# Kernel tuning notes

Hardware: AMD Instinct MI355X
Metric: run time of the kernel (lower is better)

The kernel has to match this reference:

```python
import jax, jax.numpy as jnp
import numpy as np

B, T, C = 8, 4096, 1024
NH = 64          # module sets self.n_head = dim_head = 64
HD = C // NH     # 16


def setup_inputs() -> dict:
    key = jax.random.key(0)
    ks = jax.random.split(key, 9)
    s = 1.0 / np.sqrt(C).astype(np.float32)
    x = jax.random.normal(ks[0], (B, T, C), jnp.float32)
    Wq = jax.random.normal(ks[1], (C, C), jnp.float32) * s
    bq = jax.random.normal(ks[2], (C,), jnp.float32) * 0.01
    Wk = jax.random.normal(ks[3], (C, C), jnp.float32) * s
    bk = jax.random.normal(ks[4], (C,), jnp.float32) * 0.01
    Wv = jax.random.normal(ks[5], (C, C), jnp.float32) * s
    bv = jax.random.normal(ks[6], (C,), jnp.float32) * 0.01
    Wp = jax.random.normal(ks[7], (C, C), jnp.float32) * s
    bp = jax.random.normal(ks[8], (C,), jnp.float32) * 0.01
    return {"x": x, "Wq": Wq, "bq": bq, "Wk": Wk, "bk": bk,
            "Wv": Wv, "bv": bv, "Wp": Wp, "bp": bp}


def _heads(t):
    # [B, T, C] -> [B, NH, T, HD]
    return t.reshape(B, T, NH, HD).transpose(0, 2, 1, 3)


def reference(x, Wq, bq, Wk, bk, Wv, bv, Wp, bp):
    # self-attention path: y = x; kv_mask=None (masked path is unreachable in source)
    q = _heads(x @ Wq.T + bq)
    k = _heads(x @ Wk.T + bk)
    v = _heads(x @ Wv.T + bv)
    q = jax.nn.softmax(q, axis=-1)
    k = jax.nn.softmax(k, axis=-1)
    k_cumsum = k.sum(axis=2, keepdims=True)               # [B, NH, 1, HD]
    D_inv = 1.0 / (q * k_cumsum).sum(axis=-1, keepdims=True)  # [B, NH, T, 1]
    context = jnp.einsum('bhtd,bhte->bhde', k, v)          # [B, NH, HD, HD]
    y = jnp.einsum('bhtd,bhde->bhte', q, context) * D_inv  # [B, NH, T, HD]
    y = y.transpose(0, 2, 1, 3).reshape(B, T, C)           # b h n d -> b n (h d)
    return y @ Wp.T + bp
```

## Files before the change

kernel.cpp:

```cpp
#include <hip/hip_runtime.h>
#include <stdint.h>


typedef __attribute__((ext_vector_type(8))) __bf16 bf16x8;
typedef __attribute__((ext_vector_type(4))) float f32x4;
typedef __attribute__((ext_vector_type(4))) unsigned int u32x4;
typedef __attribute__((ext_vector_type(4))) unsigned short u16x4;

#define AS1 __attribute__((address_space(1)))
#define AS3 __attribute__((address_space(3)))

__device__ __forceinline__ unsigned short f2bf(float f) {
  unsigned int u = __builtin_bit_cast(unsigned int, f);
  u += 0x7FFFu + ((u >> 16) & 1u);
  return (unsigned short)(u >> 16);
}

__device__ __forceinline__ void gl_lds16(const unsigned short* g, unsigned short* l) {
  __builtin_amdgcn_global_load_lds((const AS1 unsigned int*)g, (AS3 unsigned int*)l, 16, 0, 0);
}

__global__ __launch_bounds__(256)
void cvt_x(const float* __restrict__ src, unsigned short* __restrict__ dst, int n4) {
  int i = blockIdx.x * blockDim.x + threadIdx.x;
  const int stride = gridDim.x * blockDim.x;
  for (; i < n4; i += stride) {
    f32x4 v = *(const f32x4*)(src + (size_t)i * 4);
    u16x4 o;
    o.x = f2bf(v.x); o.y = f2bf(v.y); o.z = f2bf(v.z); o.w = f2bf(v.w);
    *(u16x4*)(dst + (size_t)i * 4) = o;
  }
}

__global__ __launch_bounds__(256)
void cvt_w(const float* __restrict__ w0, const float* __restrict__ w1,
           const float* __restrict__ w2, const float* __restrict__ w3,
           unsigned short* __restrict__ dst) {
  const int j = blockIdx.x * 256 + threadIdx.x;
  const float* ws[4] = {w0, w1, w2, w3};
  #pragma unroll
  for (int r = 0; r < 4; ++r) {
    f32x4 v = *(const f32x4*)(ws[r] + (size_t)j * 4);
    u16x4 o;
    o.x = f2bf(v.x); o.y = f2bf(v.y); o.z = f2bf(v.z); o.w = f2bf(v.w);
    *(u16x4*)(dst + ((size_t)r * 262144 + j) * 4) = o;
  }
}

template<int KIND>
__global__ __launch_bounds__(256, 3)
void gemm_pipe(const unsigned short* __restrict__ A,
               const unsigned short* __restrict__ W,
               const float* __restrict__ b0, const float* __restrict__ b1,
               const float* __restrict__ b2,
               unsigned short* __restrict__ oq, unsigned short* __restrict__ okT,
               unsigned short* __restrict__ ovT, float* __restrict__ of)
{
  __shared__ __align__(16) unsigned short lds[24576];

  const int tid  = threadIdx.x;
  const int lane = tid & 63;
  const int wid  = tid >> 6;

  const int flat  = blockIdx.x;
  const int xcd   = flat & 7;
  const int i     = flat >> 3;
  const int bcg   = i >> 8;
  const int r     = i & 255;
  const int panel = r >> 3;
  const int c     = r & 7;
  const int brow  = (xcd * 32 + panel) * 128;
  const int bcol  = (bcg * 8 + c) * 128;

  const int srow = wid * 16 + (lane >> 2);
  const int scol = ((lane & 3) ^ ((lane >> 3) & 3)) << 3;
  const unsigned short* a_src = A + (size_t)(brow + srow) * 1024 + scol;
  const unsigned short* b_src = W + (size_t)(bcol + srow) * 1024 + scol;
  unsigned short* Ldst = lds + wid * 512;

  const int wm = (wid >> 1) * 64;
  const int wn = (wid & 1) * 64;
  const int fr = lane & 15;
  const int fg = lane >> 4;
  const int sw = ((fg ^ ((fr >> 1) & 3)) << 3);
  const int aoff = (wm + fr) * 32 + sw;
  const int boff = 4096 + (wn + fr) * 32 + sw;

  const f32x4 fz = {0.f, 0.f, 0.f, 0.f};
  f32x4 acc[4][4];
  #pragma unroll
  for (int mt = 0; mt < 4; ++mt)
    #pragma unroll
    for (int nt = 0; nt < 4; ++nt) acc[mt][nt] = fz;

  auto stage = [&](int t, int buf) {
    unsigned short* d = Ldst + buf * 8192;
    const unsigned short* ga = a_src + t * 32;
    const unsigned short* gb = b_src + t * 32;
    gl_lds16(ga,         d);
    gl_lds16(ga + 65536, d + 2048);
    gl_lds16(gb,         d + 4096);
    gl_lds16(gb + 65536, d + 6144);
  };

  stage(0, 0);
  stage(1, 1);
  stage(2, 2);
  asm volatile("s_waitcnt vmcnt(8)" ::: "memory");
  __builtin_amdgcn_sched_barrier(0);
  __builtin_amdgcn_s_barrier();

  int buf = 0;
  for (int t = 0; t < 32; ++t) {
    const unsigned short* Lb = lds + buf * 8192;
    bf16x8 af[4], bfr[4];
    #pragma unroll
    for (int mt = 0; mt < 4; ++mt)
      af[mt] = __builtin_bit_cast(bf16x8, *(const u32x4*)&Lb[aoff + mt * 512]);
    #pragma unroll
    for (int nt = 0; nt < 4; ++nt)
      bfr[nt] = __builtin_bit_cast(bf16x8, *(const u32x4*)&Lb[boff + nt * 512]);
    asm volatile("s_waitcnt lgkmcnt(0)" ::: "memory");
    __builtin_amdgcn_sched_barrier(0);
    __builtin_amdgcn_s_barrier();
    if (t < 29) stage(t + 3, buf);

    __builtin_amdgcn_s_setprio(1);
    #pragma unroll
    for (int mt = 0; mt < 4; ++mt)
      #pragma unroll
      for (int nt = 0; nt < 4; ++nt)
        acc[mt][nt] = __builtin_amdgcn_mfma_f32_16x16x32_bf16(af[mt], bfr[nt], acc[mt][nt], 0, 0, 0);
    __builtin_amdgcn_s_setprio(0);

    if (t < 29) {
      asm volatile("s_waitcnt vmcnt(8)" ::: "memory");
      __builtin_amdgcn_sched_barrier(0);
      __builtin_amdgcn_s_barrier();
    } else if (t == 29) {
      asm volatile("s_waitcnt vmcnt(4)" ::: "memory");
      __builtin_amdgcn_sched_barrier(0);
      __builtin_amdgcn_s_barrier();
    } else if (t == 30) {
      asm volatile("s_waitcnt vmcnt(0)" ::: "memory");
      __builtin_amdgcn_sched_barrier(0);
      __builtin_amdgcn_s_barrier();
    }
    buf = (buf == 2) ? 0 : buf + 1;
  }

  const int sec = (KIND == 0) ? (bcol >> 10) : 0;
  const float* bias = (KIND == 1) ? b0 : (sec == 0 ? b0 : (sec == 1 ? b1 : b2));

  #pragma unroll
  for (int nt = 0; nt < 4; ++nt) {
    const int n_glob = bcol + wn + nt * 16 + fr;
    const int nn = (KIND == 0) ? (n_glob & 1023) : n_glob;
    const float bv = bias[nn];
    #pragma unroll
    for (int mt = 0; mt < 4; ++mt) {
      const int m0 = brow + wm + mt * 16 + fg * 4;
      float vals[4];
      #pragma unroll
      for (int r2 = 0; r2 < 4; ++r2) vals[r2] = acc[mt][nt][r2] + bv;

      if (KIND == 0 && sec <= 1) {
        #pragma unroll
        for (int r2 = 0; r2 < 4; ++r2) {
          float x = vals[r2];
          float mx = x;
          #pragma unroll
          for (int s = 1; s < 16; s <<= 1) mx = fmaxf(mx, __shfl_xor(mx, s, 64));
          float e = __expf(x - mx);
          float sm = e;
          #pragma unroll
          for (int s = 1; s < 16; s <<= 1) sm += __shfl_xor(sm, s, 64);
          vals[r2] = e / sm;
        }
      }

      if (KIND == 1) {
        #pragma unroll
        for (int r2 = 0; r2 < 4; ++r2)
          of[(size_t)(m0 + r2) * 1024 + n_glob] = vals[r2];
      } else if (sec == 0) {
        #pragma unroll
        for (int r2 = 0; r2 < 4; ++r2)
          oq[(size_t)(m0 + r2) * 1024 + nn] = f2bf(vals[r2]);
      } else {
        unsigned short* o = (sec == 1) ? okT : ovT;
        const int bb = m0 >> 12;
        const int t0 = m0 & 4095;
        const int hh = nn >> 4;
        const int dd = nn & 15;
        u16x4 pk;
        pk.x = f2bf(vals[0]); pk.y = f2bf(vals[1]);
        pk.z = f2bf(vals[2]); pk.w = f2bf(vals[3]);
        *(u16x4*)&o[(((size_t)bb * 64 + hh) * 16 + dd) * 4096 + t0] = pk;
      }
    }
  }
}

__global__ __launch_bounds__(256)
void attn_kernel(const unsigned short* __restrict__ qb,
                 const unsigned short* __restrict__ kT,
                 const unsigned short* __restrict__ vT,
                 unsigned short* __restrict__ yb)
{
  const int head = blockIdx.x;
  const int tid  = threadIdx.x;
  const int lane = tid & 63;
  const int wid  = tid >> 6;
  const int fr   = lane & 15;
  const int fg   = lane >> 4;

  const unsigned short* kTh = kT + (size_t)head * 16 * 4096;
  const unsigned short* vTh = vT + (size_t)head * 16 * 4096;

  const u32x4 uz = {0u, 0u, 0u, 0u};
  const f32x4 fz = {0.f, 0.f, 0.f, 0.f};
  const u32x4 uo = {0x3F803F80u, 0x3F803F80u, 0x3F803F80u, 0x3F803F80u};
  const bf16x8 ones = __builtin_bit_cast(bf16x8, uo);

  f32x4 cctx = fz, ckc = fz;
  #pragma unroll 4
  for (int t0 = wid * 1024; t0 < (wid + 1) * 1024; t0 += 32) {
    bf16x8 ak = __builtin_bit_cast(bf16x8, *(const u32x4*)&kTh[(size_t)fr * 4096 + t0 + fg * 8]);
    bf16x8 bv = __builtin_bit_cast(bf16x8, *(const u32x4*)&vTh[(size_t)fr * 4096 + t0 + fg * 8]);
    cctx = __builtin_amdgcn_mfma_f32_16x16x32_bf16(ak, bv, cctx, 0, 0, 0);
    ckc  = __builtin_amdgcn_mfma_f32_16x16x32_bf16(ak, ones, ckc, 0, 0, 0);
  }

  __shared__ float red[4][16][16];
  __shared__ float kcr[4][16];
  __shared__ float ctxf[16][16];
  __shared__ float kcf[16];

  #pragma unroll
  for (int r = 0; r < 4; ++r) red[wid][fg * 4 + r][fr] = cctx[r];
  if (fr == 0) {
    #pragma unroll
    for (int r = 0; r < 4; ++r) kcr[wid][fg * 4 + r] = ckc[r];
  }
  __syncthreads();
  {
    const int d = tid >> 4, e = tid & 15;
    ctxf[d][e] = red[0][d][e] + red[1][d][e] + red[2][d][e] + red[3][d][e];
    if (tid < 16) kcf[tid] = kcr[0][tid] + kcr[1][tid] + kcr[2][tid] + kcr[3][tid];
  }
  __syncthreads();

  bf16x8 bctx = __builtin_bit_cast(bf16x8, uz);
  bf16x8 bkc  = __builtin_bit_cast(bf16x8, uz);
  if (fg < 2) {
    #pragma unroll
    for (int j = 0; j < 8; ++j) {
      const int d = fg * 8 + j;
      bctx[j] = (__bf16)ctxf[d][fr];
      bkc[j]  = (__bf16)kcf[d];
    }
  }

  const int b = head >> 6;
  const int h = head & 63;
  const size_t qbase = (size_t)b * 4096 * 1024 + (size_t)h * 16;

  for (int step = 0; step < 64; ++step) {
    const int t0 = step * 64 + wid * 16;
    bf16x8 af = __builtin_bit_cast(bf16x8, uz);
    if (fg < 2)
      af = __builtin_bit_cast(bf16x8, *(const u32x4*)&qb[qbase + (size_t)(t0 + fr) * 1024 + fg * 8]);
    f32x4 cy = __builtin_amdgcn_mfma_f32_16x16x32_bf16(af, bctx, fz, 0, 0, 0);
    f32x4 cd = __builtin_amdgcn_mfma_f32_16x16x32_bf16(af, bkc,  fz, 0, 0, 0);
    #pragma unroll
    for (int r = 0; r < 4; ++r) {
      const int t = t0 + fg * 4 + r;
      const float yv = cy[r] * __builtin_amdgcn_rcpf(cd[r]);
      yb[qbase + (size_t)t * 1024 + fr] = f2bf(yv);
    }
  }
}

extern "C" void kernel_launch(void* const* d_in, const int* in_sizes, int n_in,
                              void* d_out, int out_size, void* d_ws, size_t ws_size,
                              hipStream_t stream)
{
  (void)in_sizes; (void)n_in; (void)out_size; (void)ws_size;
  const float* x  = (const float*)d_in[0];
  const float* Wq = (const float*)d_in[1];
  const float* bq = (const float*)d_in[2];
  const float* Wk = (const float*)d_in[3];
  const float* bk = (const float*)d_in[4];
  const float* Wv = (const float*)d_in[5];
  const float* bv = (const float*)d_in[6];
  const float* Wp = (const float*)d_in[7];
  const float* bp = (const float*)d_in[8];

  char* ws = (char*)d_ws;
  unsigned short* xb  = (unsigned short*)(ws);
  unsigned short* wb  = (unsigned short*)(ws + 67108864);
  unsigned short* qb  = (unsigned short*)(ws + 75497472);
  unsigned short* kTb = (unsigned short*)(ws + 142606336);
  unsigned short* vTb = (unsigned short*)(ws + 209715200);

  cvt_x<<<2048, 256, 0, stream>>>(x, xb, 33554432 / 4);
  cvt_w<<<1024, 256, 0, stream>>>(Wq, Wk, Wv, Wp, wb);

  gemm_pipe<0><<<6144, 256, 0, stream>>>(xb, wb, bq, bk, bv, qb, kTb, vTb, nullptr);

  attn_kernel<<<512, 256, 0, stream>>>(qb, kTb, vTb, xb );

  gemm_pipe<1><<<2048, 256, 0, stream>>>(xb , wb + 3145728, bp, bp, bp,
                                         nullptr, nullptr, nullptr, (float*)d_out);
}
```

Baseline: 529.0 us.

## Pre-swizzle weights into MFMA fragment layout and load B directly to registers

The weight conversion kernel now writes bf16 weights in a per-lane MFMA fragment order, so each wave can load its B fragments straight from global memory into registers. These loads are double-buffered across iterations. Only the A operand is still staged through LDS, which halves LDS usage and removes the B LDS reads. The trade-off is extra global/L2 traffic for B, since each wave fetches its own fragments without LDS sharing. The change also adds an extra barrier per iteration and reworks the vmcnt waits.

```diff
diff --git a/kernel.cpp b/kernel.cpp
--- a/kernel.cpp
+++ b/kernel.cpp
@@ -36,27 +36,35 @@
 void cvt_w(const float* __restrict__ w0, const float* __restrict__ w1,
            const float* __restrict__ w2, const float* __restrict__ w3,
            unsigned short* __restrict__ dst) {
-  const int j = blockIdx.x * 256 + threadIdx.x;
+  const int g = blockIdx.x * 256 + threadIdx.x;
+  const int w = g >> 17;
+  const int r = g & 131071;
+  const int f = r >> 6;
+  const int l = r & 63;
+  const int n = (f >> 5) * 16 + (l & 15);
+  const int k = (f & 31) * 32 + (l >> 4) * 8;
   const float* ws[4] = {w0, w1, w2, w3};
-  #pragma unroll
-  for (int r = 0; r < 4; ++r) {
-    f32x4 v = *(const f32x4*)(ws[r] + (size_t)j * 4);
-    u16x4 o;
-    o.x = f2bf(v.x); o.y = f2bf(v.y); o.z = f2bf(v.z); o.w = f2bf(v.w);
-    *(u16x4*)(dst + ((size_t)r * 262144 + j) * 4) = o;
-  }
+  const float* src = ws[w] + (size_t)n * 1024 + k;
+  f32x4 v0 = *(const f32x4*)src;
+  f32x4 v1 = *(const f32x4*)(src + 4);
+  u16x4 a, b;
+  a.x = f2bf(v0.x); a.y = f2bf(v0.y); a.z = f2bf(v0.z); a.w = f2bf(v0.w);
+  b.x = f2bf(v1.x); b.y = f2bf(v1.y); b.z = f2bf(v1.z); b.w = f2bf(v1.w);
+  unsigned short* o = dst + (size_t)g * 8;
+  *(u16x4*)o = a;
+  *(u16x4*)(o + 4) = b;
 }
 
 template<int KIND>
 __global__ __launch_bounds__(256, 3)
 void gemm_pipe(const unsigned short* __restrict__ A,
-               const unsigned short* __restrict__ W,
+               const unsigned short* __restrict__ Wf,
                const float* __restrict__ b0, const float* __restrict__ b1,
                const float* __restrict__ b2,
                unsigned short* __restrict__ oq, unsigned short* __restrict__ okT,
                unsigned short* __restrict__ ovT, float* __restrict__ of)
 {
-  __shared__ __align__(16) unsigned short lds[24576];
+  __shared__ __align__(16) unsigned short lds[12288];
 
   const int tid  = threadIdx.x;
   const int lane = tid & 63;
@@ -75,16 +83,15 @@
   const int srow = wid * 16 + (lane >> 2);
   const int scol = ((lane & 3) ^ ((lane >> 3) & 3)) << 3;
   const unsigned short* a_src = A + (size_t)(brow + srow) * 1024 + scol;
-  const unsigned short* b_src = W + (size_t)(bcol + srow) * 1024 + scol;
   unsigned short* Ldst = lds + wid * 512;
 
   const int wm = (wid >> 1) * 64;
   const int wn = (wid & 1) * 64;
   const int fr = lane & 15;
   const int fg = lane >> 4;
-  const int sw = ((fg ^ ((fr >> 1) & 3)) << 3);
-  const int aoff = (wm + fr) * 32 + sw;
-  const int boff = 4096 + (wn + fr) * 32 + sw;
+  const int aoff = (wm + fr) * 32 + ((fg ^ ((fr >> 1) & 3)) << 3);
+
+  const unsigned short* wfp = Wf + ((size_t)((bcol + wn) >> 4) * 32) * 512 + lane * 8;
 
   const f32x4 fz = {0.f, 0.f, 0.f, 0.f};
   f32x4 acc[4][4];
@@ -94,59 +101,53 @@
     for (int nt = 0; nt < 4; ++nt) acc[mt][nt] = fz;
 
   auto stage = [&](int t, int buf) {
-    unsigned short* d = Ldst + buf * 8192;
-    const unsigned short* ga = a_src + t * 32;
-    const unsigned short* gb = b_src + t * 32;
-    gl_lds16(ga,         d);
-    gl_lds16(ga + 65536, d + 2048);
-    gl_lds16(gb,         d + 4096);
-    gl_lds16(gb + 65536, d + 6144);
+    unsigned short* d = Ldst + buf * 4096;
+    gl_lds16(a_src + t * 32, d);
+    gl_lds16(a_src + t * 32 + 65536, d + 2048);
   };
-
-  stage(0, 0);
-  stage(1, 1);
-  stage(2, 2);
-  asm volatile("s_waitcnt vmcnt(8)" ::: "memory");
+  auto loadB = [&](int t, bf16x8 (&dst)[4]) {
+    #pragma unroll
+    for (int nt = 0; nt < 4; ++nt)
+      dst[nt] = __builtin_bit_cast(bf16x8,
+        *(const u32x4*)(wfp + (size_t)t * 512 + (size_t)nt * 16384));
+  };
+
+  bf16x8 brgA[4], brgB[4];
+
+  loadB(0, brgA);
+  stage(0, 0); stage(1, 1); stage(2, 2);
+  asm volatile("s_waitcnt vmcnt(4)" ::: "memory");
   __builtin_amdgcn_sched_barrier(0);
   __builtin_amdgcn_s_barrier();
 
-  int buf = 0;
-  for (int t = 0; t < 32; ++t) {
-    const unsigned short* Lb = lds + buf * 8192;
-    bf16x8 af[4], bfr[4];
+  auto body = [&](int t, bf16x8 (&bc)[4], bf16x8 (&bn)[4]) {
+    const unsigned short* Lb = lds + (t % 3) * 4096;
+    bf16x8 af[4];
     #pragma unroll
     for (int mt = 0; mt < 4; ++mt)
       af[mt] = __builtin_bit_cast(bf16x8, *(const u32x4*)&Lb[aoff + mt * 512]);
-    #pragma unroll
-    for (int nt = 0; nt < 4; ++nt)
-      bfr[nt] = __builtin_bit_cast(bf16x8, *(const u32x4*)&Lb[boff + nt * 512]);
     asm volatile("s_waitcnt lgkmcnt(0)" ::: "memory");
     __builtin_amdgcn_sched_barrier(0);
     __builtin_amdgcn_s_barrier();
-    if (t < 29) stage(t + 3, buf);
-
+    if (t + 3 < 32) stage(t + 3, t % 3);
+    if (t + 1 < 32) loadB(t + 1, bn);
+    if (t <= 28)      asm volatile("s_waitcnt vmcnt(6)" ::: "memory");
+    else if (t <= 30) asm volatile("s_waitcnt vmcnt(4)" ::: "memory");
+    else              asm volatile("s_waitcnt vmcnt(0)" ::: "memory");
+    __builtin_amdgcn_sched_barrier(0);
     __builtin_amdgcn_s_setprio(1);
     #pragma unroll
     for (int mt = 0; mt < 4; ++mt)
       #pragma unroll
       for (int nt = 0; nt < 4; ++nt)
-        acc[mt][nt] = __builtin_amdgcn_mfma_f32_16x16x32_bf16(af[mt], bfr[nt], acc[mt][nt], 0, 0, 0);
+        acc[mt][nt] = __builtin_amdgcn_mfma_f32_16x16x32_bf16(af[mt], bc[nt], acc[mt][nt], 0, 0, 0);
     __builtin_amdgcn_s_setprio(0);
-
-    if (t < 29) {
-      asm volatile("s_waitcnt vmcnt(8)" ::: "memory");
-      __builtin_amdgcn_sched_barrier(0);
-      __builtin_amdgcn_s_barrier();
-    } else if (t == 29) {
-      asm volatile("s_waitcnt vmcnt(4)" ::: "memory");
-      __builtin_amdgcn_sched_barrier(0);
-      __builtin_amdgcn_s_barrier();
-    } else if (t == 30) {
-      asm volatile("s_waitcnt vmcnt(0)" ::: "memory");
-      __builtin_amdgcn_sched_barrier(0);
-      __builtin_amdgcn_s_barrier();
-    }
-    buf = (buf == 2) ? 0 : buf + 1;
+    __builtin_amdgcn_s_barrier();
+  };
+
+  for (int t = 0; t < 32; t += 2) {
+    body(t,     brgA, brgB);
+    body(t + 1, brgB, brgA);
   }
 
   const int sec = (KIND == 0) ? (bcol >> 10) : 0;
@@ -305,7 +306,7 @@
   unsigned short* vTb = (unsigned short*)(ws + 209715200);
 
   cvt_x<<<2048, 256, 0, stream>>>(x, xb, 33554432 / 4);
-  cvt_w<<<1024, 256, 0, stream>>>(Wq, Wk, Wv, Wp, wb);
+  cvt_w<<<2048, 256, 0, stream>>>(Wq, Wk, Wv, Wp, wb);
 
   gemm_pipe<0><<<6144, 256, 0, stream>>>(xb, wb, bq, bk, bv, qb, kTb, vTb, nullptr);
 
```

Result: faster. 507.8 us (-4.0%).
